# Performance work log

Hardware: AMD Instinct MI355X
Metric: run time of the kernel (lower is better)

## Reference

```python
import jax, jax.numpy as jnp
import numpy as np
from math import lgamma

# dims (match init_kwargs / input_specs)
N_MELS = 80; MEM_DIM = 256; PRE1 = 256; PRE2 = 128
ATTN_LSTM = 256; ATTN_DIM = 128; S_FILT = 8; S_K = 21; D_FILT = 8; D_K = 21
P_LEN = 11; ALPHA = 0.1; BETA = 0.9; DEC_LSTM = 256; R = 2
B = 32; T_MELS = 400; T_ENC = 200


def _betabinom_prior():
    # beta-binomial pmf over [0, P_LEN-1] with n = P_LEN-1, a=ALPHA, b=BETA
    n = P_LEN - 1
    def pmf(k):
        return np.exp(lgamma(n + 1) - lgamma(k + 1) - lgamma(n - k + 1)
                      + lgamma(k + ALPHA) + lgamma(n - k + BETA) - lgamma(n + ALPHA + BETA)
                      - (lgamma(ALPHA) + lgamma(BETA) - lgamma(ALPHA + BETA)))
    return np.array([pmf(k) for k in range(P_LEN)], dtype=np.float32)


def setup_inputs() -> dict:
    ks = iter(jax.random.split(jax.random.key(0), 40))
    def w(*shape):
        return jax.random.normal(next(ks), shape, jnp.float32) / float(np.sqrt(shape[-1]))
    inp = {}
    inp["mels"] = jax.random.normal(next(ks), (B, N_MELS, T_MELS), jnp.float32)
    inp["memory"] = jax.random.normal(next(ks), (B, T_ENC, MEM_DIM), jnp.float32)
    # prenet
    inp["pre_W1"] = w(PRE1, N_MELS); inp["pre_b1"] = jnp.zeros((PRE1,), jnp.float32)
    inp["pre_W2"] = w(PRE2, PRE1); inp["pre_b2"] = jnp.zeros((PRE2,), jnp.float32)
    # attention LSTMCell (input = prenet[-1] + memory_dim)
    inp["al_Wih"] = w(4 * ATTN_LSTM, PRE2 + MEM_DIM); inp["al_Whh"] = w(4 * ATTN_LSTM, ATTN_LSTM)
    inp["al_bih"] = jnp.zeros((4 * ATTN_LSTM,), jnp.float32); inp["al_bhh"] = jnp.zeros((4 * ATTN_LSTM,), jnp.float32)
    # dynamic convolution attention
    inp["att_W"] = w(ATTN_DIM, ATTN_LSTM); inp["att_Wb"] = jnp.zeros((ATTN_DIM,), jnp.float32)
    inp["att_V"] = w(D_FILT * D_K, ATTN_DIM)
    inp["att_F"] = w(S_FILT, 1, S_K)
    inp["att_U"] = w(ATTN_DIM, S_FILT)
    inp["att_T"] = w(ATTN_DIM, D_FILT); inp["att_Tb"] = jnp.zeros((ATTN_DIM,), jnp.float32)
    inp["att_v"] = w(ATTN_DIM)
    inp["prior"] = jnp.asarray(_betabinom_prior())
    # decoder LSTMCell (input = attn_lstm_size + memory_dim)
    inp["dl_Wih"] = w(4 * DEC_LSTM, ATTN_LSTM + MEM_DIM); inp["dl_Whh"] = w(4 * DEC_LSTM, DEC_LSTM)
    inp["dl_bih"] = jnp.zeros((4 * DEC_LSTM,), jnp.float32); inp["dl_bhh"] = jnp.zeros((4 * DEC_LSTM,), jnp.float32)
    # acoustic projection
    inp["ac_W"] = w(N_MELS * R, DEC_LSTM + MEM_DIM); inp["ac_b"] = jnp.zeros((N_MELS * R,), jnp.float32)
    return inp


def _forward(mels, memory, pre_W1, pre_b1, pre_W2, pre_b2,
             al_Wih, al_Whh, al_bih, al_bhh,
             att_W, att_Wb, att_V, att_F, att_U, att_T, att_Tb, att_v, prior,
             dl_Wih, dl_Whh, dl_bih, dl_bhh, ac_W, ac_b):
    Bq = mels.shape[0]
    dn = ('NCH', 'OIH', 'NCH')
    prior_k = prior[::-1][None, None, :]  # torch registers flipped prior as conv kernel

    def lstm(x, h, c, Wih, Whh, bih, bhh):
        gates = x @ Wih.T + bih + h @ Whh.T + bhh
        i, f, g, o = jnp.split(gates, 4, axis=-1)
        c_new = jax.nn.sigmoid(f) * c + jax.nn.sigmoid(i) * jnp.tanh(g)
        return jax.nn.sigmoid(o) * jnp.tanh(c_new), c_new

    def dca(query, align):
        # query [B, attn_lstm], align [B, T_enc]
        T = align.shape[-1]
        # causal prior convolution, log-clamped
        p = jax.lax.conv_general_dilated(align[:, None, :], prior_k, (1,), [(P_LEN - 1, 0)], dimension_numbers=dn)[:, 0]
        p = jnp.log(jnp.clip(p, 1e-6))
        # per-example dynamic filters G: [B, C*K]
        G = jnp.tanh(query @ att_W.T + att_Wb) @ att_V.T
        g = jax.lax.conv_general_dilated(align[None, :, :], G.reshape(Bq * D_FILT, 1, D_K), (1,),
                                         [((D_K - 1) // 2,) * 2], dimension_numbers=dn,
                                         feature_group_count=Bq)[0].reshape(Bq, D_FILT, T)
        # static filters: [B, S, T]
        f = jax.lax.conv_general_dilated(align[:, None, :], att_F, (1,), [((S_K - 1) // 2,) * 2], dimension_numbers=dn)
        e = jnp.tanh(jnp.einsum('bst,as->bta', f, att_U) + jnp.einsum('bct,ac->bta', g, att_T) + att_Tb) @ att_v
        return jax.nn.softmax(e + p, axis=-1)

    def step(carry, x):
        align, ctx, h1, c1, h2, c2 = carry
        # prenet (dropout disabled: eval-mode deterministic reference)
        pre = jax.nn.relu(jax.nn.relu(x @ pre_W1.T + pre_b1) @ pre_W2.T + pre_b2)
        h1, c1 = lstm(jnp.concatenate([ctx, pre], -1), h1, c1, al_Wih, al_Whh, al_bih, al_bhh)
        align = dca(h1, align)
        ctx = jnp.einsum('bt,btd->bd', align, memory)
        h2, c2 = lstm(jnp.concatenate([h1, ctx], -1), h2, c2, dl_Wih, dl_Whh, dl_bih, dl_bhh)
        out = (jnp.concatenate([h2, ctx], -1) @ ac_W.T + ac_b).reshape(Bq, N_MELS, R)
        return (align, ctx, h1, c1, h2, c2), (out, align)

    T_enc = memory.shape[1]
    align0 = jnp.zeros((Bq, T_enc), jnp.float32).at[:, 0].set(1.0)  # one-hot at position 0
    carry0 = (align0,
              jnp.zeros((Bq, MEM_DIM), jnp.float32),
              jnp.zeros((Bq, ATTN_LSTM), jnp.float32), jnp.zeros((Bq, ATTN_LSTM), jnp.float32),
              jnp.zeros((Bq, DEC_LSTM), jnp.float32), jnp.zeros((Bq, DEC_LSTM), jnp.float32))
    # teacher forcing: step t>0 consumes ground-truth frame mels[:, :, t-1] for t in range(0, T, R)
    frames = jnp.moveaxis(mels[:, :, R - 1::R], 2, 0)  # [steps, B, N]
    xs = jnp.concatenate([jnp.zeros((1, Bq, N_MELS), jnp.float32), frames[:-1]], axis=0)
    _, (outs, aligns) = jax.lax.scan(step, carry0, xs)
    output_mels = jnp.moveaxis(outs, 0, 2).reshape(Bq, N_MELS, -1)  # cat along time: [B, N, T]
    alignments = jnp.moveaxis(aligns, 0, 2)  # stack dim=2: [B, T_enc, steps]
    return output_mels, alignments


def reference(mels, memory, pre_W1, pre_b1, pre_W2, pre_b2,
              al_Wih, al_Whh, al_bih, al_bhh,
              att_W, att_Wb, att_V, att_F, att_U, att_T, att_Tb, att_v, prior,
              dl_Wih, dl_Whh, dl_bih, dl_bhh, ac_W, ac_b):
    return _forward(mels, memory, pre_W1, pre_b1, pre_W2, pre_b2,
                    al_Wih, al_Whh, al_bih, al_bhh,
                    att_W, att_Wb, att_V, att_F, att_U, att_T, att_Tb, att_v, prior,
                    dl_Wih, dl_Whh, dl_bih, dl_bhh, ac_W, ac_b)
```

## Files before the change

### kernel.cpp

```cpp
#include <hip/hip_runtime.h>
#include <math.h>

#define BB 32
#define TENC 200
#define NMELS 80
#define TMELS 400
#define STEPS 200
#define MEM 256
#define PRE1N 256
#define PRE2N 128
#define AD 128
#define DK 21
#define DF 8
#define SK 21
#define SF 8
#define PL 11
#define BLK 1024

#define QW1 0u
#define QW2 655360u
#define HP5 1441792u
#define WS_ATTWT 761856u
#define WS_PW1T  816128u
#define WS_PW2T  836608u
#define WS_PRE2  869376u
#define WS_MEMH  1688576u
#define WS_AVTH  2507776u

#define L_XS   0
#define L_H1   768
#define L_C1   1024
#define L_H2   1280
#define L_C2   1536
#define L_CTX  1792
#define L_AL   2048
#define L_PS   2248
#define L_ES   2448
#define L_P4   2656
#define L_QS   6752
#define L_GS   6880
#define L_FS   7048
#define L_WF   8648
#define L_PR   8816
#define L_RB   8828
#define L_B1   8848
#define L_B2   9872
#define L_AW   10896
#define DYNF   27280
#define DYNB   (DYNF*4)

__device__ __forceinline__ float sigm(float x){ return 1.f/(1.f+expf(-x)); }
__device__ __forceinline__ float tanh_fast(float x){
  float ax = fabsf(x);
  float z = __expf(-2.f*ax);
  float r = (1.f - z)/(1.f + z);
  return (x < 0.f) ? -r : r;
}
__device__ __forceinline__ unsigned short to_bf16(float f){
  unsigned u = __float_as_uint(f);
  return (unsigned short)((u + 0x7fffu + ((u>>16)&1u)) >> 16);
}

#define FMA8S(wv, xa, xb, acc) \
  acc += __uint_as_float((wv).x<<16)*(xa).x + __uint_as_float((wv).x&0xffff0000u)*(xa).y \
       + __uint_as_float((wv).y<<16)*(xa).z + __uint_as_float((wv).y&0xffff0000u)*(xa).w \
       + __uint_as_float((wv).z<<16)*(xb).x + __uint_as_float((wv).z&0xffff0000u)*(xb).y \
       + __uint_as_float((wv).w<<16)*(xb).z + __uint_as_float((wv).w&0xffff0000u)*(xb).w;
#define FMA8(wv, xp, a0, a1, a2, a3) \
  a0 += __uint_as_float((wv).x << 16)*(xp)[0] + __uint_as_float((wv).x & 0xffff0000u)*(xp)[1]; \
  a1 += __uint_as_float((wv).y << 16)*(xp)[2] + __uint_as_float((wv).y & 0xffff0000u)*(xp)[3]; \
  a2 += __uint_as_float((wv).z << 16)*(xp)[4] + __uint_as_float((wv).z & 0xffff0000u)*(xp)[5]; \
  a3 += __uint_as_float((wv).w << 16)*(xp)[6] + __uint_as_float((wv).w & 0xffff0000u)*(xp)[7];

__global__ __launch_bounds__(256) void trk(const float* __restrict__ s, float* __restrict__ d, int R, int C){
  int i = blockIdx.x*256 + threadIdx.x;
  if (i < R*C){ int r = i / C, c = i - r*C; d[c*R + r] = s[i]; }
}
__global__ __launch_bounds__(256) void pkq1c(const float* __restrict__ wih, const float* __restrict__ whh,
                                             unsigned short* __restrict__ d){
  int i = blockIdx.x*256 + threadIdx.x;
  if (i < 1024*640){
    int c = i / 640, k = i - c*640;
    float v = (k < 384) ? wih[c*384 + k] : whh[c*256 + (k-384)];
    int q = k / 160, kr = k - 160*q, kk = kr >> 3, e = kr & 7;
    d[((unsigned)((q*20 + kk)*1024 + c))*8u + e] = to_bf16(v);
  }
}
__global__ __launch_bounds__(256) void pkq2c(const float* __restrict__ wih, const float* __restrict__ whh,
                                             unsigned short* __restrict__ d){
  int i = blockIdx.x*256 + threadIdx.x;
  if (i < 1024*768){
    int c = i / 768, k = i - c*768;
    float v = (k < 512) ? wih[c*512 + k] : whh[c*256 + (k-512)];
    int q = k / 192, kr = k - 192*q, kk = kr >> 3, e = kr & 7;
    d[((unsigned)((q*24 + kk)*1024 + c))*8u + e] = to_bf16(v);
  }
}
__global__ __launch_bounds__(256) void pk8h(const float* __restrict__ s, unsigned short* __restrict__ d, int R, int C){
  int i = blockIdx.x*256 + threadIdx.x;
  if (i < R*C){ int r = i / C, c = i - r*C; d[(unsigned)(c>>3)*(unsigned)R*8u + (unsigned)r*8u + (c&7)] = to_bf16(s[i]); }
}
__global__ __launch_bounds__(256) void pkmem(const float* __restrict__ s, unsigned short* __restrict__ d, int n){
  int i = blockIdx.x*256 + threadIdx.x;
  if (i < n) d[i] = to_bf16(s[i]);
}
__global__ __launch_bounds__(256) void pkavt(const float* __restrict__ s, unsigned short* __restrict__ d){
  int i = blockIdx.x*256 + threadIdx.x;
  if (i < 128*168){ int k = i/168, a = i - k*168; d[i] = to_bf16(s[a*128 + k]); }
}

__global__ __launch_bounds__(256) void prenetk(const float* __restrict__ mels,
    const float* __restrict__ b1, const float* __restrict__ b2, float* __restrict__ ws){
  int t = blockIdx.x, tid = threadIdx.x;
  __shared__ float xS[BB*NMELS];
  __shared__ float p1S[BB*PRE1N];
  const float* W1T = ws + WS_PW1T;
  const float* W2T = ws + WS_PW2T;
  for (int i=tid;i<BB*NMELS;i+=256){
    int r = i/NMELS, k = i - r*NMELS;
    xS[i] = (t==0)?0.f : mels[r*NMELS*TMELS + k*TMELS + (2*t-1)];
  }
  __syncthreads();
  {
    float acc[BB];
    #pragma unroll
    for (int r=0;r<BB;r++) acc[r]=0.f;
    for (int k=0;k<NMELS;k++){
      float w = W1T[k*PRE1N + tid];
      #pragma unroll
      for (int r=0;r<BB;r++) acc[r] += xS[r*NMELS+k]*w;
    }
    float bb = b1[tid];
    #pragma unroll
    for (int r=0;r<BB;r++) p1S[r*PRE1N+tid] = fmaxf(acc[r]+bb, 0.f);
  }
  __syncthreads();
  if (tid < PRE2N){
    float acc[BB];
    #pragma unroll
    for (int r=0;r<BB;r++) acc[r]=0.f;
    for (int k=0;k<PRE1N;k++){
      float w = W2T[k*PRE2N + tid];
      #pragma unroll
      for (int r=0;r<BB;r++) acc[r] += p1S[r*PRE1N+k]*w;
    }
    float bb = b2[tid];
    #pragma unroll
    for (int r=0;r<BB;r++) ws[WS_PRE2 + ((unsigned)t*BB + r)*PRE2N + tid] = fmaxf(acc[r]+bb, 0.f);
  }
}

__global__ __launch_bounds__(BLK) void decoder(
    const float* __restrict__ albih, const float* __restrict__ albhh,
    const float* __restrict__ dlbih, const float* __restrict__ dlbhh,
    const float* __restrict__ prior, const float* __restrict__ attF,
    const float* __restrict__ attWb, const float* __restrict__ attU,
    const float* __restrict__ attT, const float* __restrict__ attTb,
    const float* __restrict__ attv,
    const float* __restrict__ acb, const float* __restrict__ ws,
    float* __restrict__ out){
  extern __shared__ float sm[];
  const int b = blockIdx.x, tid = threadIdx.x;
  unsigned short* aWh = (unsigned short*)(sm + L_AW);
  const unsigned* aWu = (const unsigned*)(sm + L_AW);

  if (tid < 256){ sm[L_H1+tid]=0.f; sm[L_C1+tid]=0.f; sm[L_H2+tid]=0.f; sm[L_C2+tid]=0.f; sm[L_CTX+tid]=0.f; }
  if (tid < TENC) sm[L_AL+tid] = (tid==0)?1.f:0.f;
  sm[L_B1+tid] = albih[tid] + albhh[tid];
  sm[L_B2+tid] = dlbih[tid] + dlbhh[tid];
  if (tid < SF*SK) sm[L_WF+tid] = attF[tid];
  if (tid < PL)    sm[L_PR+tid] = prior[tid];
  for (int i = tid; i < 32768; i += BLK) aWh[i] = to_bf16(ws[WS_ATTWT + i]);
  __syncthreads();

  const unsigned short* hw = (const unsigned short*)ws;
  const unsigned short* Q1 = hw + QW1;
  const unsigned short* Q2 = hw + QW2;
  const unsigned short* P5 = hw + HP5;
  const unsigned* memh = (const unsigned*)(ws + WS_MEMH);
  const unsigned short* avth = (const unsigned short*)(ws + WS_AVTH);
  const float acbv  = (tid < 640) ? acb[tid >> 2] : 0.f;
  const int q = tid >> 8, c0 = tid & 255;

  for (int t = 0; t < STEPS; ++t){
    if (tid < 256) sm[L_XS+tid] = sm[L_CTX+tid];
    else if (tid < 384) sm[L_XS+tid] = __builtin_nontemporal_load(&ws[WS_PRE2 + ((unsigned)t*BB + b)*PRE2N + (tid-256)]);
    else if (tid < 640) sm[L_XS+tid] = sm[L_H1 + (tid-384)];
    __syncthreads();
    {
      const float* xq = sm + L_XS + 160*q;
      const unsigned short* Wq = Q1 + (unsigned)q*163840u;
      float a0=0.f, a1=0.f, a2=0.f, a3=0.f;
      #pragma unroll 4
      for (int kk = 0; kk < 20; kk++){
        float4 xa = *(const float4*)(xq + 8*kk);
        float4 xb = *(const float4*)(xq + 8*kk + 4);
        const unsigned short* wr = Wq + (unsigned)kk*8192u + c0*8u;
        uint4 w0 = *(const uint4*)(wr);
        uint4 w1 = *(const uint4*)(wr + 2048);
        uint4 w2 = *(const uint4*)(wr + 4096);
        uint4 w3 = *(const uint4*)(wr + 6144);
        FMA8S(w0, xa, xb, a0)
        FMA8S(w1, xa, xb, a1)
        FMA8S(w2, xa, xb, a2)
        FMA8S(w3, xa, xb, a3)
      }
      sm[L_P4 + q*1024 + c0      ] = a0;
      sm[L_P4 + q*1024 + c0 + 256] = a1;
      sm[L_P4 + q*1024 + c0 + 512] = a2;
      sm[L_P4 + q*1024 + c0 + 768] = a3;
    }
    __syncthreads();
    if (tid < 256){
      float g[4];
      #pragma unroll
      for (int gg2 = 0; gg2 < 4; gg2++){
        int col = gg2*256 + tid;
        g[gg2] = sm[L_B1+col] + sm[L_P4+col] + sm[L_P4+1024+col] + sm[L_P4+2048+col] + sm[L_P4+3072+col];
      }
      float c = sigm(g[1])*sm[L_C1+tid] + sigm(g[0])*tanhf(g[2]);
      sm[L_C1+tid] = c;
      sm[L_H1+tid] = sigm(g[3])*tanhf(c);
    }
    __syncthreads();
    if (tid < 512){
      const int quarter = tid >> 7, a = tid & 127;
      const int sel = a & 1, au = a >> 1;
      float s = 0.f;
      for (int k = 64*quarter; k < 64*quarter+64; k++){
        unsigned u = aWu[k*64 + au];
        float wv = __uint_as_float(sel ? (u & 0xffff0000u) : (u << 16));
        s += sm[L_H1+k]*wv;
      }
      sm[L_P4 + tid] = s;
    } else if (tid < 512+TENC){
      const int pos = tid - 512;
      float s = 0.f;
      #pragma unroll
      for (int jj = 0; jj < PL; jj++){ int qq = pos - jj; if (qq >= 0) s += sm[L_PR+jj]*sm[L_AL+qq]; }
      sm[L_PS+pos] = logf(fmaxf(s, 1e-6f));
      #pragma unroll
      for (int c = 0; c < SF; c++){
        float s2 = 0.f;
        #pragma unroll
        for (int k = 0; k < SK; k++){ int qq = pos + k - 10; if (qq>=0 && qq<TENC) s2 += sm[L_WF+c*SK+k]*sm[L_AL+qq]; }
        sm[L_FS + c*TENC + pos] = s2;
      }
    }
    __syncthreads();
    if (tid < AD) sm[L_QS+tid] = tanhf(attWb[tid] + sm[L_P4+tid] + sm[L_P4+128+tid] + sm[L_P4+256+tid] + sm[L_P4+384+tid]);
    __syncthreads();
    if (tid < DF*DK){
      float a = 0.f;
      for (int k = 0; k < AD; k++) a += sm[L_QS+k]*__uint_as_float(((unsigned)avth[k*(DF*DK)+tid])<<16);
      sm[L_GS+tid] = a;
    }
    __syncthreads();
    if (tid < 4*TENC){
      const int pos = tid >> 2, qr = tid & 3;
      float g[DF];
      #pragma unroll
      for (int c=0;c<DF;c++){
        float s=0.f;
        #pragma unroll
        for (int k=0;k<DK;k++){
          int q2 = pos + k - 10;
          if (q2>=0 && q2<TENC) s += sm[L_AL+q2]*sm[L_GS+c*DK+k];
        }
        g[c]=s;
      }
      float fv[SF];
      #pragma unroll
      for (int s2=0;s2<SF;s2++) fv[s2] = sm[L_FS + s2*TENC + pos];
      float pp = 0.f;
      for (int h = qr*32; h < qr*32+32; h++){
        float u = attTb[h];
        #pragma unroll
        for (int s2=0;s2<SF;s2++) u += attU[h*SF+s2]*fv[s2];
        #pragma unroll
        for (int c=0;c<DF;c++) u += attT[h*DF+c]*g[c];
        pp += attv[h]*tanh_fast(u);
      }
      pp += __shfl_xor(pp,1);
      pp += __shfl_xor(pp,2);
      if (qr==0) sm[L_ES+pos] = pp + sm[L_PS+pos];
    }
    __syncthreads();
    float ex;
    {
      float v = (tid<TENC)? sm[L_ES+tid] : -3.0e38f;
      for (int o=1;o<64;o<<=1) v = fmaxf(v, __shfl_xor(v,o));
      if ((tid&63)==0) sm[L_RB+(tid>>6)] = v;
      __syncthreads();
      if (tid==0){ sm[L_RB+16] = fmaxf(fmaxf(sm[L_RB],sm[L_RB+1]), fmaxf(sm[L_RB+2],sm[L_RB+3])); }
      __syncthreads();
      float m = sm[L_RB+16];
      ex = (tid<TENC)? expf(sm[L_ES+tid]-m) : 0.f;
      float sv = ex;
      for (int o=1;o<64;o<<=1) sv += __shfl_xor(sv,o);
      __syncthreads();
      if ((tid&63)==0) sm[L_RB+(tid>>6)] = sv;
      __syncthreads();
      if (tid==0){ sm[L_RB+16] = 1.f/(sm[L_RB]+sm[L_RB+1]+sm[L_RB+2]+sm[L_RB+3]); }
      __syncthreads();
      float inv = sm[L_RB+16];
      if (tid<TENC){
        float a = ex*inv;
        sm[L_AL+tid] = a;
        out[1024000 + b*TENC*STEPS + tid*STEPS + t] = a;
      }
    }
    __syncthreads();
    {
      const int grp2 = tid >> 7, jp = tid & 127;
      const unsigned base = ((unsigned)b*TENC)*128u + jp;
      float a0 = 0.f, a1 = 0.f;
      for (int p = grp2*25; p < grp2*25+25; p++){
        unsigned u = memh[base + (unsigned)p*128u];
        float al = sm[L_AL+p];
        a0 += al*__uint_as_float(u << 16);
        a1 += al*__uint_as_float(u & 0xffff0000u);
      }
      sm[L_P4 + grp2*256 + 2*jp    ] = a0;
      sm[L_P4 + grp2*256 + 2*jp + 1] = a1;
    }
    __syncthreads();
    if (tid < 256){
      float c = 0.f;
      #pragma unroll
      for (int g2 = 0; g2 < 8; g2++) c += sm[L_P4 + g2*256 + tid];
      sm[L_CTX+tid] = c;
      sm[L_XS+256+tid] = c;
    } else if (tid < 512){
      sm[L_XS + (tid-256)] = sm[L_H1 + (tid-256)];
    } else if (tid < 768){
      sm[L_XS + tid] = sm[L_H2 + (tid-512)];
    }
    __syncthreads();
    {
      const float* xq = sm + L_XS + 192*q;
      const unsigned short* Wq = Q2 + (unsigned)q*196608u;
      float a0=0.f, a1=0.f, a2=0.f, a3=0.f;
      #pragma unroll 4
      for (int kk = 0; kk < 24; kk++){
        float4 xa = *(const float4*)(xq + 8*kk);
        float4 xb = *(const float4*)(xq + 8*kk + 4);
        const unsigned short* wr = Wq + (unsigned)kk*8192u + c0*8u;
        uint4 w0 = *(const uint4*)(wr);
        uint4 w1 = *(const uint4*)(wr + 2048);
        uint4 w2 = *(const uint4*)(wr + 4096);
        uint4 w3 = *(const uint4*)(wr + 6144);
        FMA8S(w0, xa, xb, a0)
        FMA8S(w1, xa, xb, a1)
        FMA8S(w2, xa, xb, a2)
        FMA8S(w3, xa, xb, a3)
      }
      sm[L_P4 + q*1024 + c0      ] = a0;
      sm[L_P4 + q*1024 + c0 + 256] = a1;
      sm[L_P4 + q*1024 + c0 + 512] = a2;
      sm[L_P4 + q*1024 + c0 + 768] = a3;
    }
    __syncthreads();
    if (tid < 256){
      float g[4];
      #pragma unroll
      for (int gg2 = 0; gg2 < 4; gg2++){
        int col = gg2*256 + tid;
        g[gg2] = sm[L_B2+col] + sm[L_P4+col] + sm[L_P4+1024+col] + sm[L_P4+2048+col] + sm[L_P4+3072+col];
      }
      float c = sigm(g[1])*sm[L_C2+tid] + sigm(g[0])*tanhf(g[2]);
      sm[L_C2+tid] = c;
      sm[L_H2+tid] = sigm(g[3])*tanhf(c);
    }
    __syncthreads();
    if (tid < 640){
      const int col = tid >> 2, qq = tid & 3;
      float a0 = 0.f, a1 = 0.f, a2 = 0.f, a3 = 0.f;
      #pragma unroll 4
      for (int kk = qq*16; kk < qq*16+16; kk++){
        uint4 wv = *(const uint4*)(P5 + (unsigned)kk*1280u + col*8u);
        const float* xp = (kk < 32) ? (sm + L_H2 + 8*kk) : (sm + L_CTX + 8*kk - 256);
        FMA8(wv, xp, a0, a1, a2, a3)
      }
      float acc = (a0+a1)+(a2+a3);
      acc += __shfl_xor(acc,1);
      acc += __shfl_xor(acc,2);
      if (qq==0){
        const int m = col >> 1, r = col & 1;
        out[(unsigned)b*NMELS*TMELS + m*TMELS + 2*t + r] = acc + acbv;
      }
    }
    __syncthreads();
  }
}

extern "C" void kernel_launch(void* const* d_in, const int* in_sizes, int n_in,
                              void* d_out, int out_size, void* d_ws, size_t ws_size,
                              hipStream_t stream) {
  (void)in_sizes; (void)n_in; (void)out_size; (void)ws_size;
  const float* mels   = (const float*)d_in[0];
  const float* memory = (const float*)d_in[1];
  const float* pre_W1 = (const float*)d_in[2];
  const float* pre_b1 = (const float*)d_in[3];
  const float* pre_W2 = (const float*)d_in[4];
  const float* pre_b2 = (const float*)d_in[5];
  const float* al_Wih = (const float*)d_in[6];
  const float* al_Whh = (const float*)d_in[7];
  const float* al_bih = (const float*)d_in[8];
  const float* al_bhh = (const float*)d_in[9];
  const float* att_W  = (const float*)d_in[10];
  const float* att_Wb = (const float*)d_in[11];
  const float* att_V  = (const float*)d_in[12];
  const float* att_F  = (const float*)d_in[13];
  const float* att_U  = (const float*)d_in[14];
  const float* att_T  = (const float*)d_in[15];
  const float* att_Tb = (const float*)d_in[16];
  const float* att_v  = (const float*)d_in[17];
  const float* prior  = (const float*)d_in[18];
  const float* dl_Wih = (const float*)d_in[19];
  const float* dl_Whh = (const float*)d_in[20];
  const float* dl_bih = (const float*)d_in[21];
  const float* dl_bhh = (const float*)d_in[22];
  const float* ac_W   = (const float*)d_in[23];
  const float* ac_b   = (const float*)d_in[24];
  float* ws  = (float*)d_ws;
  unsigned short* hw = (unsigned short*)d_ws;
  float* out = (float*)d_out;

  hipFuncSetAttribute((const void*)decoder, hipFuncAttributeMaxDynamicSharedMemorySize, DYNB);

  auto TR = [&](const float* src, unsigned off, int R, int C){
    int n = R*C;
    trk<<<dim3((n+255)/256), dim3(256), 0, stream>>>(src, ws + off, R, C);
  };
  pkq1c<<<dim3((1024*640+255)/256), dim3(256), 0, stream>>>(al_Wih, al_Whh, hw + QW1);
  pkq2c<<<dim3((1024*768+255)/256), dim3(256), 0, stream>>>(dl_Wih, dl_Whh, hw + QW2);
  pk8h<<<dim3((160*512+255)/256), dim3(256), 0, stream>>>(ac_W, hw + HP5, 160, 512);
  TR(att_W,  WS_ATTWT, 128, 256);
  TR(pre_W1, WS_PW1T,  256, 80);
  TR(pre_W2, WS_PW2T,  128, 256);
  {
    int n = BB*TENC*MEM;
    pkmem<<<dim3((n+255)/256), dim3(256), 0, stream>>>(memory, (unsigned short*)(ws + WS_MEMH), n);
  }
  pkavt<<<dim3((128*168+255)/256), dim3(256), 0, stream>>>(att_V, (unsigned short*)(ws + WS_AVTH));

  prenetk<<<dim3(STEPS), dim3(256), 0, stream>>>(mels, pre_b1, pre_b2, ws);

  decoder<<<dim3(BB), dim3(BLK), DYNB, stream>>>(
      al_bih, al_bhh, dl_bih, dl_bhh, prior, att_F,
      att_Wb, att_U, att_T, att_Tb, att_v,
      ac_b, ws, out);
}
```

Baseline: 26.00 ms.

## Defer mel projection to next step and fold input staging into previous barrier phase

The acoustic projection for step t-1 now runs on otherwise idle threads (712-871) during the step-t attention/prior phase, and the last step's projection moves after the loop. Staging of the next step's LSTM input vector is merged into the decoder-LSTM phase, and the softmax is reduced to a single wavefront. Together these remove several block-wide barriers per step from the serial 200-step recurrence. The cost is extra per-thread work in the projection (one thread per column over all 64 k-chunks instead of four-way split with shuffles) and some added index logic.

```diff
diff --git a/kernel.cpp b/kernel.cpp
--- a/kernel.cpp
+++ b/kernel.cpp
@@ -66,11 +66,6 @@
        + __uint_as_float((wv).y<<16)*(xa).z + __uint_as_float((wv).y&0xffff0000u)*(xa).w \
        + __uint_as_float((wv).z<<16)*(xb).x + __uint_as_float((wv).z&0xffff0000u)*(xb).y \
        + __uint_as_float((wv).w<<16)*(xb).z + __uint_as_float((wv).w&0xffff0000u)*(xb).w;
-#define FMA8(wv, xp, a0, a1, a2, a3) \
-  a0 += __uint_as_float((wv).x << 16)*(xp)[0] + __uint_as_float((wv).x & 0xffff0000u)*(xp)[1]; \
-  a1 += __uint_as_float((wv).y << 16)*(xp)[2] + __uint_as_float((wv).y & 0xffff0000u)*(xp)[3]; \
-  a2 += __uint_as_float((wv).z << 16)*(xp)[4] + __uint_as_float((wv).z & 0xffff0000u)*(xp)[5]; \
-  a3 += __uint_as_float((wv).w << 16)*(xp)[6] + __uint_as_float((wv).w & 0xffff0000u)*(xp)[7];
 
 __global__ __launch_bounds__(256) void trk(const float* __restrict__ s, float* __restrict__ d, int R, int C){
   int i = blockIdx.x*256 + threadIdx.x;
@@ -164,7 +159,12 @@
   unsigned short* aWh = (unsigned short*)(sm + L_AW);
   const unsigned* aWu = (const unsigned*)(sm + L_AW);
 
-  if (tid < 256){ sm[L_H1+tid]=0.f; sm[L_C1+tid]=0.f; sm[L_H2+tid]=0.f; sm[L_C2+tid]=0.f; sm[L_CTX+tid]=0.f; }
+  if (tid < 256){
+    sm[L_H1+tid]=0.f; sm[L_C1+tid]=0.f; sm[L_H2+tid]=0.f; sm[L_C2+tid]=0.f; sm[L_CTX+tid]=0.f;
+    sm[L_XS+tid]=0.f;
+    sm[L_XS+384+tid]=0.f;
+  }
+  if (tid >= 256 && tid < 384) sm[L_XS+tid] = ws[WS_PRE2 + ((unsigned)0*BB + b)*PRE2N + (tid-256)];
   if (tid < TENC) sm[L_AL+tid] = (tid==0)?1.f:0.f;
   sm[L_B1+tid] = albih[tid] + albhh[tid];
   sm[L_B2+tid] = dlbih[tid] + dlbhh[tid];
@@ -179,14 +179,9 @@
   const unsigned short* P5 = hw + HP5;
   const unsigned* memh = (const unsigned*)(ws + WS_MEMH);
   const unsigned short* avth = (const unsigned short*)(ws + WS_AVTH);
-  const float acbv  = (tid < 640) ? acb[tid >> 2] : 0.f;
   const int q = tid >> 8, c0 = tid & 255;
 
   for (int t = 0; t < STEPS; ++t){
-    if (tid < 256) sm[L_XS+tid] = sm[L_CTX+tid];
-    else if (tid < 384) sm[L_XS+tid] = __builtin_nontemporal_load(&ws[WS_PRE2 + ((unsigned)t*BB + b)*PRE2N + (tid-256)]);
-    else if (tid < 640) sm[L_XS+tid] = sm[L_H1 + (tid-384)];
-    __syncthreads();
     {
       const float* xq = sm + L_XS + 160*q;
       const unsigned short* Wq = Q1 + (unsigned)q*163840u;
@@ -246,6 +241,28 @@
         for (int k = 0; k < SK; k++){ int qq = pos + k - 10; if (qq>=0 && qq<TENC) s2 += sm[L_WF+c*SK+k]*sm[L_AL+qq]; }
         sm[L_FS + c*TENC + pos] = s2;
       }
+    } else if (tid < 872){
+      if (t >= 1){
+        const int col = tid - 712;
+        float a0=0.f, a1=0.f, a2=0.f, a3=0.f;
+        #pragma unroll 4
+        for (int kk = 0; kk < 64; kk += 4){
+          const float* xp0 = (kk   < 32) ? (sm + L_H2 + 8*kk)        : (sm + L_CTX + 8*kk - 256);
+          const float* xp1 = (kk+1 < 32) ? (sm + L_H2 + 8*(kk+1))    : (sm + L_CTX + 8*(kk+1) - 256);
+          const float* xp2 = (kk+2 < 32) ? (sm + L_H2 + 8*(kk+2))    : (sm + L_CTX + 8*(kk+2) - 256);
+          const float* xp3 = (kk+3 < 32) ? (sm + L_H2 + 8*(kk+3))    : (sm + L_CTX + 8*(kk+3) - 256);
+          uint4 w0 = *(const uint4*)(P5 + (unsigned)(kk  )*1280u + col*8u);
+          uint4 w1 = *(const uint4*)(P5 + (unsigned)(kk+1)*1280u + col*8u);
+          uint4 w2 = *(const uint4*)(P5 + (unsigned)(kk+2)*1280u + col*8u);
+          uint4 w3 = *(const uint4*)(P5 + (unsigned)(kk+3)*1280u + col*8u);
+          FMA8S(w0, *(const float4*)xp0, *(const float4*)(xp0+4), a0)
+          FMA8S(w1, *(const float4*)xp1, *(const float4*)(xp1+4), a1)
+          FMA8S(w2, *(const float4*)xp2, *(const float4*)(xp2+4), a2)
+          FMA8S(w3, *(const float4*)xp3, *(const float4*)(xp3+4), a3)
+        }
+        const int m = col >> 1, r = col & 1;
+        out[(unsigned)b*NMELS*TMELS + m*TMELS + 2*(t-1) + r] = (a0+a1)+(a2+a3) + acb[col];
+      }
     }
     __syncthreads();
     if (tid < AD) sm[L_QS+tid] = tanhf(attWb[tid] + sm[L_P4+tid] + sm[L_P4+128+tid] + sm[L_P4+256+tid] + sm[L_P4+384+tid]);
@@ -286,28 +303,26 @@
       if (qr==0) sm[L_ES+pos] = pp + sm[L_PS+pos];
     }
     __syncthreads();
-    float ex;
-    {
-      float v = (tid<TENC)? sm[L_ES+tid] : -3.0e38f;
-      for (int o=1;o<64;o<<=1) v = fmaxf(v, __shfl_xor(v,o));
-      if ((tid&63)==0) sm[L_RB+(tid>>6)] = v;
-      __syncthreads();
-      if (tid==0){ sm[L_RB+16] = fmaxf(fmaxf(sm[L_RB],sm[L_RB+1]), fmaxf(sm[L_RB+2],sm[L_RB+3])); }
-      __syncthreads();
-      float m = sm[L_RB+16];
-      ex = (tid<TENC)? expf(sm[L_ES+tid]-m) : 0.f;
-      float sv = ex;
+    if (tid < 64){
+      float v0 = sm[L_ES+tid], v1 = sm[L_ES+64+tid], v2 = sm[L_ES+128+tid];
+      float v3 = (tid < 8) ? sm[L_ES+192+tid] : -3.0e38f;
+      float mx = fmaxf(fmaxf(v0,v1), fmaxf(v2,v3));
+      for (int o=1;o<64;o<<=1) mx = fmaxf(mx, __shfl_xor(mx,o));
+      float e0 = expf(v0-mx), e1 = expf(v1-mx), e2 = expf(v2-mx);
+      float e3 = (tid < 8) ? expf(v3-mx) : 0.f;
+      float sv = ((e0+e1)+(e2+e3));
       for (int o=1;o<64;o<<=1) sv += __shfl_xor(sv,o);
-      __syncthreads();
-      if ((tid&63)==0) sm[L_RB+(tid>>6)] = sv;
-      __syncthreads();
-      if (tid==0){ sm[L_RB+16] = 1.f/(sm[L_RB]+sm[L_RB+1]+sm[L_RB+2]+sm[L_RB+3]); }
-      __syncthreads();
-      float inv = sm[L_RB+16];
-      if (tid<TENC){
-        float a = ex*inv;
-        sm[L_AL+tid] = a;
-        out[1024000 + b*TENC*STEPS + tid*STEPS + t] = a;
+      float inv = 1.f/sv;
+      float a0 = e0*inv, a1 = e1*inv, a2 = e2*inv;
+      sm[L_AL+tid] = a0; sm[L_AL+64+tid] = a1; sm[L_AL+128+tid] = a2;
+      unsigned ob = 1024000u + (unsigned)b*TENC*STEPS + (unsigned)t;
+      out[ob + (unsigned)tid*STEPS]       = a0;
+      out[ob + (unsigned)(64+tid)*STEPS]  = a1;
+      out[ob + (unsigned)(128+tid)*STEPS] = a2;
+      if (tid < 8){
+        float a3 = e3*inv;
+        sm[L_AL+192+tid] = a3;
+        out[ob + (unsigned)(192+tid)*STEPS] = a3;
       }
     }
     __syncthreads();
@@ -371,26 +386,36 @@
       float c = sigm(g[1])*sm[L_C2+tid] + sigm(g[0])*tanhf(g[2]);
       sm[L_C2+tid] = c;
       sm[L_H2+tid] = sigm(g[3])*tanhf(c);
-    }
-    __syncthreads();
-    if (tid < 640){
-      const int col = tid >> 2, qq = tid & 3;
-      float a0 = 0.f, a1 = 0.f, a2 = 0.f, a3 = 0.f;
-      #pragma unroll 4
-      for (int kk = qq*16; kk < qq*16+16; kk++){
-        uint4 wv = *(const uint4*)(P5 + (unsigned)kk*1280u + col*8u);
-        const float* xp = (kk < 32) ? (sm + L_H2 + 8*kk) : (sm + L_CTX + 8*kk - 256);
-        FMA8(wv, xp, a0, a1, a2, a3)
-      }
-      float acc = (a0+a1)+(a2+a3);
-      acc += __shfl_xor(acc,1);
-      acc += __shfl_xor(acc,2);
-      if (qq==0){
-        const int m = col >> 1, r = col & 1;
-        out[(unsigned)b*NMELS*TMELS + m*TMELS + 2*t + r] = acc + acbv;
-      }
-    }
-    __syncthreads();
+    } else if (tid < 384){
+      if (t+1 < STEPS)
+        sm[L_XS+tid] = __builtin_nontemporal_load(&ws[WS_PRE2 + ((unsigned)(t+1)*BB + b)*PRE2N + (tid-256)]);
+    } else if (tid < 640){
+      sm[L_XS+tid] = sm[L_H1 + (tid-384)];
+    } else if (tid < 896){
+      sm[L_XS + (tid-640)] = sm[L_CTX + (tid-640)];
+    }
+    __syncthreads();
+  }
+  if (tid < 160){
+    const int col = tid;
+    float a0=0.f, a1=0.f, a2=0.f, a3=0.f;
+    #pragma unroll 4
+    for (int kk = 0; kk < 64; kk += 4){
+      const float* xp0 = (kk   < 32) ? (sm + L_H2 + 8*kk)     : (sm + L_CTX + 8*kk - 256);
+      const float* xp1 = (kk+1 < 32) ? (sm + L_H2 + 8*(kk+1)) : (sm + L_CTX + 8*(kk+1) - 256);
+      const float* xp2 = (kk+2 < 32) ? (sm + L_H2 + 8*(kk+2)) : (sm + L_CTX + 8*(kk+2) - 256);
+      const float* xp3 = (kk+3 < 32) ? (sm + L_H2 + 8*(kk+3)) : (sm + L_CTX + 8*(kk+3) - 256);
+      uint4 w0 = *(const uint4*)(P5 + (unsigned)(kk  )*1280u + col*8u);
+      uint4 w1 = *(const uint4*)(P5 + (unsigned)(kk+1)*1280u + col*8u);
+      uint4 w2 = *(const uint4*)(P5 + (unsigned)(kk+2)*1280u + col*8u);
+      uint4 w3 = *(const uint4*)(P5 + (unsigned)(kk+3)*1280u + col*8u);
+      FMA8S(w0, *(const float4*)xp0, *(const float4*)(xp0+4), a0)
+      FMA8S(w1, *(const float4*)xp1, *(const float4*)(xp1+4), a1)
+      FMA8S(w2, *(const float4*)xp2, *(const float4*)(xp2+4), a2)
+      FMA8S(w3, *(const float4*)xp3, *(const float4*)(xp3+4), a3)
+    }
+    const int m = col >> 1, r = col & 1;
+    out[(unsigned)b*NMELS*TMELS + m*TMELS + 2*(STEPS-1) + r] = (a0+a1)+(a2+a3) + acb[col];
   }
 }
 
```

New measurement: 23.41 ms. -10.0%, faster.
